# Kernel tuning notes

Hardware: AMD Instinct MI355X
Metric: run time of the kernel (lower is better)

## Reference

```python
import jax, jax.numpy as jnp
import numpy as np

K = 3          # kernel size (implied by 18/27 offset channels)
PAD = 1
STRIDE = 1


def setup_inputs() -> dict:
    key = jax.random.key(0)
    k0, k1, k2 = jax.random.split(key, 3)
    B, C, H, W = 4, 256, 64, 64
    Cout = 256
    x = jax.random.normal(k0, (B, C, H, W), jnp.float32)
    # offset/mask predicting conv: 18 offset + 9 mask channels (deform_group=1)
    w_off = jax.random.normal(k1, (27, C, K, K), jnp.float32) * 0.01
    b_off = jnp.zeros((27,), jnp.float32)
    # main deformable conv weight (bias=False)
    w = jax.random.normal(k2, (Cout, C, K, K), jnp.float32) * 0.05
    return {"x": x, "w_off": w_off, "b_off": b_off, "w": w}


def _modulated_dcn(x, w_off, b_off, w):
    B, C, H, W = x.shape
    KK = K * K
    # regular conv predicting offsets (+ mask)
    om = jax.lax.conv_general_dilated(
        x, w_off, (STRIDE, STRIDE), [(PAD, PAD), (PAD, PAD)],
        dimension_numbers=("NCHW", "OIHW", "NCHW")) + b_off[None, :, None, None]
    Ho, Wo = om.shape[2], om.shape[3]
    # channel layout: interleaved (dy, dx) per kernel tap, then 9 mask channels
    off = om[:, :2 * KK].reshape(B, KK, 2, Ho, Wo)
    mask = jax.nn.sigmoid(om[:, 2 * KK:3 * KK])            # (B, KK, Ho, Wo)

    ky, kx = jnp.meshgrid(jnp.arange(K), jnp.arange(K), indexing="ij")
    base_y = (jnp.arange(Ho) * STRIDE - PAD)[:, None]       # (Ho, 1)
    base_x = (jnp.arange(Wo) * STRIDE - PAD)[None, :]       # (1, Wo)
    # sampling positions p = p0 + pn + offset, shape (B, KK, Ho, Wo)
    py = base_y[None, None] + ky.reshape(KK)[None, :, None, None] + off[:, :, 0]
    px = base_x[None, None] + kx.reshape(KK)[None, :, None, None] + off[:, :, 1]

    y0f = jnp.floor(py)
    x0f = jnp.floor(px)
    ly = py - y0f
    lx = px - x0f
    y0 = y0f.astype(jnp.int32)
    x0 = x0f.astype(jnp.int32)

    xf = x.reshape(B, C, H * W)

    def samp(yi, xi):
        valid = ((yi >= 0) & (yi < H) & (xi >= 0) & (xi < W)).astype(x.dtype)
        idx = jnp.clip(yi, 0, H - 1) * W + jnp.clip(xi, 0, W - 1)
        v = jnp.take_along_axis(xf, idx.reshape(B, 1, -1), axis=2)
        return v.reshape(B, C, KK, Ho, Wo) * valid[:, None]

    # bilinear interpolation with zero padding outside the image
    v = (samp(y0,     x0    ) * ((1 - ly) * (1 - lx))[:, None]
         + samp(y0,     x0 + 1) * ((1 - ly) * lx)[:, None]
         + samp(y0 + 1, x0    ) * (ly * (1 - lx))[:, None]
         + samp(y0 + 1, x0 + 1) * (ly * lx)[:, None])
    v = v * mask[:, None]                                   # modulation
    # conv as contraction over (Cin, KK)
    return jnp.einsum("bckhw,ock->bohw", v, w.reshape(w.shape[0], C, KK))


def reference(x, w_off, b_off, w):
    return _modulated_dcn(x, w_off, b_off, w)
```

## Files before the change

### kernel.cpp

```cpp
#include <hip/hip_runtime.h>
#include <math.h>

#define HH 64
#define WW 64
#define CIN 256
#define COUT 256
#define KKT 9
#define HWSZ 4096
#define VP 260
#define TP 264

typedef __bf16  v8bf   __attribute__((ext_vector_type(8)));
typedef float   v4f    __attribute__((ext_vector_type(4)));
typedef short   short8 __attribute__((ext_vector_type(8)));
typedef unsigned short ushort4v __attribute__((ext_vector_type(4)));

__device__ inline unsigned short f2bf(float f) {
    union { float f; unsigned u; } uf; uf.f = f;
    unsigned r = uf.u + 0x7fff + ((uf.u >> 16) & 1);
    return (unsigned short)(r >> 16);
}
__device__ inline float bf2f(unsigned short u) {
    union { unsigned u; float f; } uf; uf.u = ((unsigned)u) << 16;
    return uf.f;
}

__global__ __launch_bounds__(256) void k_prep(const float* __restrict__ x,
                                              const float* __restrict__ w,
                                              const float* __restrict__ w_off,
                                              unsigned short* __restrict__ x_t,
                                              unsigned short* __restrict__ wprep,
                                              unsigned short* __restrict__ woffp) {
    __shared__ __align__(16) unsigned short s_t[32 * TP];
    int id  = blockIdx.x;
    int tid = threadIdx.x;
    if (id < 512) {
        int b    = id >> 7;
        int r    = id & 127;
        int h    = r >> 1;
        int half = r & 1;
        const float* xr = x + ((size_t)b * CIN) * HWSZ + h * WW + half * 32;
#pragma unroll
        for (int it = 0; it < 8; it++) {
            int idx = it * 256 + tid;
            int c   = idx >> 3;
            int p4  = idx & 7;
            float4 v = *(const float4*)(xr + (size_t)c * HWSZ + p4 * 4);
            s_t[(p4 * 4 + 0) * TP + c] = f2bf(v.x);
            s_t[(p4 * 4 + 1) * TP + c] = f2bf(v.y);
            s_t[(p4 * 4 + 2) * TP + c] = f2bf(v.z);
            s_t[(p4 * 4 + 3) * TP + c] = f2bf(v.w);
        }
        __syncthreads();
        unsigned short* orow = x_t + (((size_t)(b * 64 + h)) * WW + half * 32) * CIN;
#pragma unroll
        for (int it = 0; it < 4; it++) {
            int idx = it * 256 + tid;
            int px  = idx >> 5;
            int c8  = (idx & 31) * 8;
            *(short8*)(orow + (size_t)px * CIN + c8) = *(const short8*)&s_t[px * TP + c8];
        }
    } else if (id < 768) {
        float* s_w = (float*)s_t;
        int o = id - 512;
        for (int i = tid; i < 2304; i += 256) s_w[i] = w[(size_t)o * 2304 + i];
        __syncthreads();
        for (int u = tid; u < 576; u += 256) {
            int t  = u >> 3;
            int kq = u & 7;
            unsigned short v[4];
#pragma unroll
            for (int j = 0; j < 4; j++) {
                int kp = t * 32 + kq * 4 + j;
                int kk = kp >> 8;
                int c  = kp & 255;
                v[j] = f2bf(s_w[c * 9 + kk]);
            }
            *(ushort4v*)&wprep[((size_t)(t * 256 + o)) * 32 + kq * 4] = *(ushort4v*)v;
        }
    } else {
        int t = id - 768;
#pragma unroll
        for (int i = 0; i < 4; i++) {
            int idx = i * 256 + tid;
            int och = idx >> 5;
            int ki  = idx & 31;
            int kp  = t * 32 + ki;
            int kk  = kp >> 8;
            int c   = kp & 255;
            float v = (och < 27) ? w_off[((size_t)och * 256 + c) * 9 + kk] : 0.f;
            woffp[(size_t)t * 1024 + idx] = f2bf(v);
        }
    }
}

__global__ __launch_bounds__(256) void k_off_mfma(const unsigned short* __restrict__ x_t,
                                                  const unsigned short* __restrict__ woffp,
                                                  const float* __restrict__ b_off,
                                                  float* __restrict__ om) {
    int id    = blockIdx.x;
    int g     = id & 7;
    int phalf = (id >> 3) & 1;
    int hi    = (id >> 4) & 7;
    int b     = id >> 7;
    int h     = g * 8 + hi;
    int p0    = phalf * 32;
    int tid  = threadIdx.x;
    int lane = tid & 63;
    int wv   = tid >> 6;
    int g2   = wv >> 1;
    int ntw  = wv & 1;
    int m16  = lane & 15;
    int quad = lane >> 4;

    __shared__ unsigned short s_row[3 * 34 * VP];
    __shared__ float s_red[2][32][33];

    const unsigned short* xb = x_t + (size_t)b * HWSZ * CIN;

    for (int u = tid; u < 3 * 1088; u += 256) {
        int row = u / 1088;
        int rem = u - row * 1088;
        int px  = rem >> 5;
        int c8  = (rem & 31) * 8;
        int y   = h + row - 1;
        int xg  = p0 + px - 1;
        short8 val = (short8)0;
        if ((unsigned)y < HH && (unsigned)xg < WW)
            val = *(const short8*)(xb + ((size_t)y * WW + xg) * CIN + c8);
        *(short8*)&s_row[(row * 34 + px) * VP + c8] = val;
    }
    __syncthreads();

    v4f acc[2];
    acc[0] = (v4f)(0.f);
    acc[1] = (v4f)(0.f);

#pragma unroll
    for (int ky = 0; ky < 3; ky++) {
#pragma unroll
        for (int kx = 0; kx < 3; kx++) {
#pragma unroll
            for (int c2 = 0; c2 < 4; c2++) {
                int ch = c2 * 2 + g2;
                int t  = (ky * 3 + kx) * 8 + ch;
                const unsigned short* wp = woffp + (size_t)t * 1024;
                short8 af0 = *(const short8*)(wp + m16 * 32 + quad * 8);
                short8 af1 = *(const short8*)(wp + (16 + m16) * 32 + quad * 8);
                short8 bfr = *(const short8*)
                    &s_row[(ky * 34 + ntw * 16 + m16 + kx) * VP + ch * 32 + quad * 8];
                acc[0] = __builtin_amdgcn_mfma_f32_16x16x32_bf16(
                    __builtin_bit_cast(v8bf, af0), __builtin_bit_cast(v8bf, bfr), acc[0], 0, 0, 0);
                acc[1] = __builtin_amdgcn_mfma_f32_16x16x32_bf16(
                    __builtin_bit_cast(v8bf, af1), __builtin_bit_cast(v8bf, bfr), acc[1], 0, 0, 0);
            }
        }
    }

#pragma unroll
    for (int mt = 0; mt < 2; mt++)
#pragma unroll
        for (int r = 0; r < 4; r++)
            s_red[g2][mt * 16 + quad * 4 + r][ntw * 16 + m16] = acc[mt][r];
    __syncthreads();

    for (int i2 = tid; i2 < 27 * 32; i2 += 256) {
        int och = i2 >> 5;
        int px  = i2 & 31;
        float s = s_red[0][och][px] + s_red[1][och][px] + b_off[och];
        om[((size_t)b * 27 + och) * HWSZ + h * WW + p0 + px] = s;
    }
}

__global__ __launch_bounds__(512, 2) void k_main(const unsigned short* __restrict__ x_t,
                                                 const float* __restrict__ om,
                                                 const unsigned short* __restrict__ wprep,
                                                 float* __restrict__ out) {
    int id = blockIdx.x;
    id = ((id & 7) << 5) | (id >> 3);
    int b  = id >> 6;
    int h  = id & 63;
    int tid  = threadIdx.x;
    int lane = tid & 63;
    int oct  = tid >> 6;
    int m16  = lane & 15;
    int quad = lane >> 4;

    __shared__ int4   s_base[KKT][64];
    __shared__ float4 s_wt  [KKT][64];
    __shared__ __align__(16) unsigned short s_v[64 * VP];

    const float* omb = om + (size_t)b * 27 * HWSZ + h * WW;
    for (int i = tid; i < KKT * 64; i += 512) {
        int kk = i >> 6;
        int pl = i & 63;
        float offy = omb[(size_t)(2 * kk)     * HWSZ + pl];
        float offx = omb[(size_t)(2 * kk + 1) * HWSZ + pl];
        float mv   = omb[(size_t)(18 + kk)    * HWSZ + pl];
        int ky = kk / 3, kx = kk - 3 * (kk / 3);
        float py = (float)(h - 1 + ky) + offy;
        float px = (float)(pl - 1 + kx) + offx;
        float y0f = floorf(py);
        float x0f = floorf(px);
        float ly = py - y0f, lx = px - x0f;
        int y0 = (int)y0f, x0 = (int)x0f;
        float m = 1.f / (1.f + __expf(-mv));
        bool yv0 = (unsigned)y0       < HH;
        bool yv1 = (unsigned)(y0 + 1) < HH;
        bool xv0 = (unsigned)x0       < WW;
        bool xv1 = (unsigned)(x0 + 1) < WW;
        int y0c = min(max(y0, 0), HH - 1);
        int y1c = min(max(y0 + 1, 0), HH - 1);
        int x0c = min(max(x0, 0), WW - 1);
        int x1c = min(max(x0 + 1, 0), WW - 1);
        s_base[kk][pl] = make_int4((y0c * WW + x0c) * CIN, (y0c * WW + x1c) * CIN,
                                   (y1c * WW + x0c) * CIN, (y1c * WW + x1c) * CIN);
        s_wt[kk][pl] = make_float4(
            (yv0 && xv0) ? (1.f - ly) * (1.f - lx) * m : 0.f,
            (yv0 && xv1) ? (1.f - ly) * lx         * m : 0.f,
            (yv1 && xv0) ? ly * (1.f - lx)         * m : 0.f,
            (yv1 && xv1) ? ly * lx                 * m : 0.f);
    }
    __syncthreads();

    v4f acc[2][4];
#pragma unroll
    for (int mt = 0; mt < 2; mt++)
#pragma unroll
        for (int nt = 0; nt < 4; nt++) acc[mt][nt] = (v4f)(0.f);

    const unsigned short* xb = x_t + (size_t)b * HWSZ * CIN;
    const unsigned short* xc = xb + lane * 4;

    for (int kk = 0; kk < KKT; kk++) {
#pragma unroll
        for (int i = 0; i < 8; i++) {
            int pl = oct * 8 + i;
            int4   bp = s_base[kk][pl];
            float4 wt = s_wt[kk][pl];
            ushort4v t0 = *(const ushort4v*)(xc + bp.x);
            ushort4v t1 = *(const ushort4v*)(xc + bp.y);
            ushort4v t2 = *(const ushort4v*)(xc + bp.z);
            ushort4v t3 = *(const ushort4v*)(xc + bp.w);
            unsigned short vv[4];
#pragma unroll
            for (int j = 0; j < 4; j++) {
                float val = wt.x * bf2f(t0[j]) + wt.y * bf2f(t1[j])
                          + wt.z * bf2f(t2[j]) + wt.w * bf2f(t3[j]);
                vv[j] = f2bf(val);
            }
            *(ushort4v*)&s_v[pl * VP + lane * 4] = *(ushort4v*)vv;
        }
        __syncthreads();

#pragma unroll 2
        for (int ch = 0; ch < 8; ch++) {
            int t = kk * 8 + ch;
            const unsigned short* wp = wprep + ((size_t)t * 256 + oct * 32) * 32;
            short8 af0 = *(const short8*)(wp + m16 * 32 + quad * 8);
            short8 af1 = *(const short8*)(wp + (16 + m16) * 32 + quad * 8);
            short8 bfr[4];
#pragma unroll
            for (int nt = 0; nt < 4; nt++)
                bfr[nt] = *(const short8*)&s_v[(nt * 16 + m16) * VP + ch * 32 + quad * 8];
#pragma unroll
            for (int nt = 0; nt < 4; nt++) {
                acc[0][nt] = __builtin_amdgcn_mfma_f32_16x16x32_bf16(
                    __builtin_bit_cast(v8bf, af0), __builtin_bit_cast(v8bf, bfr[nt]),
                    acc[0][nt], 0, 0, 0);
                acc[1][nt] = __builtin_amdgcn_mfma_f32_16x16x32_bf16(
                    __builtin_bit_cast(v8bf, af1), __builtin_bit_cast(v8bf, bfr[nt]),
                    acc[1][nt], 0, 0, 0);
            }
        }
        __syncthreads();
    }

    float* ob = out + ((size_t)b * COUT) * HWSZ + h * WW;
#pragma unroll
    for (int mt = 0; mt < 2; mt++)
#pragma unroll
        for (int nt = 0; nt < 4; nt++)
#pragma unroll
            for (int r = 0; r < 4; r++) {
                int o = oct * 32 + mt * 16 + quad * 4 + r;
                ob[(size_t)o * HWSZ + nt * 16 + m16] = acc[mt][nt][r];
            }
}

extern "C" void kernel_launch(void* const* d_in, const int* in_sizes, int n_in,
                              void* d_out, int out_size, void* d_ws, size_t ws_size,
                              hipStream_t stream) {
    const float* x     = (const float*)d_in[0];
    const float* w_off = (const float*)d_in[1];
    const float* b_off = (const float*)d_in[2];
    const float* w     = (const float*)d_in[3];
    float* out = (float*)d_out;

    float* om = (float*)d_ws;
    unsigned short* x_t   = (unsigned short*)(om + 442368);
    unsigned short* wprep = x_t + (size_t)4 * HWSZ * CIN;
    unsigned short* woffp = wprep + 589824;

    hipLaunchKernelGGL(k_prep,     dim3(840), dim3(256), 0, stream, x, w, w_off, x_t, wprep, woffp);
    hipLaunchKernelGGL(k_off_mfma, dim3(512), dim3(256), 0, stream, x_t, woffp, b_off, om);
    hipLaunchKernelGGL(k_main,     dim3(256), dim3(512), 0, stream, x_t, om, wprep, out);
}
```

Before: 146.3 us.

## Double-buffer sampled tile and prefetch next tap gathers and weight fragments

Moves the bilinear gather loads for the next kernel tap ahead of the barrier into registers and double-buffers the shared sampled tile. This removes one of the two block barriers per tap. The weight A-fragments are also prefetched one chunk ahead. The aim is to hide global gather latency behind the MFMA phase, at the cost of many more live registers (32 ushort4 values plus prefetched fragments) and double the LDS for s_v, which may lower occupancy under launch_bounds(512,2).

```diff
diff --git a/kernel.cpp b/kernel.cpp
--- a/kernel.cpp
+++ b/kernel.cpp
@@ -188,7 +188,7 @@
 
     __shared__ int4   s_base[KKT][64];
     __shared__ float4 s_wt  [KKT][64];
-    __shared__ __align__(16) unsigned short s_v[64 * VP];
+    __shared__ __align__(16) unsigned short s_v[2][64 * VP];
 
     const float* omb = om + (size_t)b * 27 * HWSZ + h * WW;
     for (int i = tid; i < KKT * 64; i += 512) {
@@ -232,48 +232,75 @@
     const unsigned short* xb = x_t + (size_t)b * HWSZ * CIN;
     const unsigned short* xc = xb + lane * 4;
 
+    ushort4v tt[8][4];
+#pragma unroll
+    for (int i = 0; i < 8; i++) {
+        int4 bp = s_base[0][oct * 8 + i];
+        tt[i][0] = *(const ushort4v*)(xc + bp.x);
+        tt[i][1] = *(const ushort4v*)(xc + bp.y);
+        tt[i][2] = *(const ushort4v*)(xc + bp.z);
+        tt[i][3] = *(const ushort4v*)(xc + bp.w);
+    }
+
+#pragma unroll
     for (int kk = 0; kk < KKT; kk++) {
+        unsigned short* sv = &s_v[kk & 1][0];
+
 #pragma unroll
         for (int i = 0; i < 8; i++) {
             int pl = oct * 8 + i;
-            int4   bp = s_base[kk][pl];
             float4 wt = s_wt[kk][pl];
-            ushort4v t0 = *(const ushort4v*)(xc + bp.x);
-            ushort4v t1 = *(const ushort4v*)(xc + bp.y);
-            ushort4v t2 = *(const ushort4v*)(xc + bp.z);
-            ushort4v t3 = *(const ushort4v*)(xc + bp.w);
             unsigned short vv[4];
 #pragma unroll
             for (int j = 0; j < 4; j++) {
-                float val = wt.x * bf2f(t0[j]) + wt.y * bf2f(t1[j])
-                          + wt.z * bf2f(t2[j]) + wt.w * bf2f(t3[j]);
+                float val = wt.x * bf2f(tt[i][0][j]) + wt.y * bf2f(tt[i][1][j])
+                          + wt.z * bf2f(tt[i][2][j]) + wt.w * bf2f(tt[i][3][j]);
                 vv[j] = f2bf(val);
             }
-            *(ushort4v*)&s_v[pl * VP + lane * 4] = *(ushort4v*)vv;
-        }
-        __syncthreads();
-
-#pragma unroll 2
+            *(ushort4v*)&sv[pl * VP + lane * 4] = *(ushort4v*)vv;
+        }
+
+        if (kk < KKT - 1) {
+#pragma unroll
+            for (int i = 0; i < 8; i++) {
+                int4 bp = s_base[kk + 1][oct * 8 + i];
+                tt[i][0] = *(const ushort4v*)(xc + bp.x);
+                tt[i][1] = *(const ushort4v*)(xc + bp.y);
+                tt[i][2] = *(const ushort4v*)(xc + bp.z);
+                tt[i][3] = *(const ushort4v*)(xc + bp.w);
+            }
+        }
+        __builtin_amdgcn_sched_barrier(0);
+        asm volatile("s_waitcnt lgkmcnt(0)" ::: "memory");
+        __builtin_amdgcn_s_barrier();
+        __builtin_amdgcn_sched_barrier(0);
+
+        const unsigned short* wpb = wprep + ((size_t)(kk * 8) * 256 + oct * 32) * 32;
+        short8 a0 = *(const short8*)(wpb + m16 * 32 + quad * 8);
+        short8 a1 = *(const short8*)(wpb + (16 + m16) * 32 + quad * 8);
+#pragma unroll
         for (int ch = 0; ch < 8; ch++) {
-            int t = kk * 8 + ch;
-            const unsigned short* wp = wprep + ((size_t)t * 256 + oct * 32) * 32;
-            short8 af0 = *(const short8*)(wp + m16 * 32 + quad * 8);
-            short8 af1 = *(const short8*)(wp + (16 + m16) * 32 + quad * 8);
+            short8 na0, na1;
+            if (ch < 7) {
+                const unsigned short* wpn = wpb + (size_t)(ch + 1) * 8192;
+                na0 = *(const short8*)(wpn + m16 * 32 + quad * 8);
+                na1 = *(const short8*)(wpn + (16 + m16) * 32 + quad * 8);
+            }
             short8 bfr[4];
 #pragma unroll
             for (int nt = 0; nt < 4; nt++)
-                bfr[nt] = *(const short8*)&s_v[(nt * 16 + m16) * VP + ch * 32 + quad * 8];
+                bfr[nt] = *(const short8*)&sv[(nt * 16 + m16) * VP + ch * 32 + quad * 8];
 #pragma unroll
             for (int nt = 0; nt < 4; nt++) {
                 acc[0][nt] = __builtin_amdgcn_mfma_f32_16x16x32_bf16(
-                    __builtin_bit_cast(v8bf, af0), __builtin_bit_cast(v8bf, bfr[nt]),
+                    __builtin_bit_cast(v8bf, a0), __builtin_bit_cast(v8bf, bfr[nt]),
                     acc[0][nt], 0, 0, 0);
                 acc[1][nt] = __builtin_amdgcn_mfma_f32_16x16x32_bf16(
-                    __builtin_bit_cast(v8bf, af1), __builtin_bit_cast(v8bf, bfr[nt]),
+                    __builtin_bit_cast(v8bf, a1), __builtin_bit_cast(v8bf, bfr[nt]),
                     acc[1][nt], 0, 0, 0);
             }
-        }
-        __syncthreads();
+            if (ch < 7) { a0 = na0; a1 = na1; }
+        }
     }
 
     float* ob = out + ((size_t)b * COUT) * HWSZ + h * WW;
```

Measured after the change: 181.3 us. 1.24x slower.

## Split k_main tiles into half-rows with 16-byte bilinear gathers

Applied to the files above, without the earlier changes.

The main deformable-conv kernel now gives each block half an output row (32 pixels) instead of a full row, doubling the grid to 512 blocks and raising the occupancy hint to 4 blocks per CU. The gather stage is restructured so each lane loads 8 bf16 channels (16 bytes) per corner and handles two pixels per tap. Block-to-(batch, row) mapping is also changed for locality. This targets the low block count on a many-CU GPU, but the weight fragments loaded from global memory are now reused across only half as many pixels, doubling that traffic and adding more per-tap barrier overhead.

```diff
diff --git a/kernel.cpp b/kernel.cpp
--- a/kernel.cpp
+++ b/kernel.cpp
@@ -14,6 +14,7 @@
 typedef float   v4f    __attribute__((ext_vector_type(4)));
 typedef short   short8 __attribute__((ext_vector_type(8)));
 typedef unsigned short ushort4v __attribute__((ext_vector_type(4)));
+typedef unsigned short ushort8v __attribute__((ext_vector_type(8)));
 
 __device__ inline unsigned short f2bf(float f) {
     union { float f; unsigned u; } uf; uf.f = f;
@@ -172,34 +173,40 @@
     }
 }
 
-__global__ __launch_bounds__(512, 2) void k_main(const unsigned short* __restrict__ x_t,
+__global__ __launch_bounds__(512, 4) void k_main(const unsigned short* __restrict__ x_t,
                                                  const float* __restrict__ om,
                                                  const unsigned short* __restrict__ wprep,
                                                  float* __restrict__ out) {
-    int id = blockIdx.x;
-    id = ((id & 7) << 5) | (id >> 3);
-    int b  = id >> 6;
-    int h  = id & 63;
+    int id    = blockIdx.x;
+    int g     = id & 7;
+    int phalf = (id >> 3) & 1;
+    int hi    = (id >> 4) & 7;
+    int b     = id >> 7;
+    int h     = g * 8 + hi;
+    int p0    = phalf * 32;
     int tid  = threadIdx.x;
     int lane = tid & 63;
     int oct  = tid >> 6;
     int m16  = lane & 15;
     int quad = lane >> 4;
-
-    __shared__ int4   s_base[KKT][64];
-    __shared__ float4 s_wt  [KKT][64];
-    __shared__ __align__(16) unsigned short s_v[64 * VP];
+    int hsel = lane >> 5;
+    int l32  = lane & 31;
+
+    __shared__ int4   s_base[KKT][32];
+    __shared__ float4 s_wt  [KKT][32];
+    __shared__ __align__(16) unsigned short s_v[32 * VP];
 
     const float* omb = om + (size_t)b * 27 * HWSZ + h * WW;
-    for (int i = tid; i < KKT * 64; i += 512) {
-        int kk = i >> 6;
-        int pl = i & 63;
-        float offy = omb[(size_t)(2 * kk)     * HWSZ + pl];
-        float offx = omb[(size_t)(2 * kk + 1) * HWSZ + pl];
-        float mv   = omb[(size_t)(18 + kk)    * HWSZ + pl];
+    for (int i = tid; i < KKT * 32; i += 512) {
+        int kk = i >> 5;
+        int pl = i & 31;
+        int p  = p0 + pl;
+        float offy = omb[(size_t)(2 * kk)     * HWSZ + p];
+        float offx = omb[(size_t)(2 * kk + 1) * HWSZ + p];
+        float mv   = omb[(size_t)(18 + kk)    * HWSZ + p];
         int ky = kk / 3, kx = kk - 3 * (kk / 3);
         float py = (float)(h - 1 + ky) + offy;
-        float px = (float)(pl - 1 + kx) + offx;
+        float px = (float)(p - 1 + kx) + offx;
         float y0f = floorf(py);
         float x0f = floorf(px);
         float ly = py - y0f, lx = px - x0f;
@@ -223,33 +230,49 @@
     }
     __syncthreads();
 
-    v4f acc[2][4];
+    v4f acc[2][2];
 #pragma unroll
     for (int mt = 0; mt < 2; mt++)
 #pragma unroll
-        for (int nt = 0; nt < 4; nt++) acc[mt][nt] = (v4f)(0.f);
+        for (int nt = 0; nt < 2; nt++) acc[mt][nt] = (v4f)(0.f);
 
     const unsigned short* xb = x_t + (size_t)b * HWSZ * CIN;
-    const unsigned short* xc = xb + lane * 4;
+    const unsigned short* xcf = xb + l32 * 8;
 
     for (int kk = 0; kk < KKT; kk++) {
-#pragma unroll
-        for (int i = 0; i < 8; i++) {
-            int pl = oct * 8 + i;
-            int4   bp = s_base[kk][pl];
-            float4 wt = s_wt[kk][pl];
-            ushort4v t0 = *(const ushort4v*)(xc + bp.x);
-            ushort4v t1 = *(const ushort4v*)(xc + bp.y);
-            ushort4v t2 = *(const ushort4v*)(xc + bp.z);
-            ushort4v t3 = *(const ushort4v*)(xc + bp.w);
-            unsigned short vv[4];
-#pragma unroll
-            for (int j = 0; j < 4; j++) {
-                float val = wt.x * bf2f(t0[j]) + wt.y * bf2f(t1[j])
-                          + wt.z * bf2f(t2[j]) + wt.w * bf2f(t3[j]);
+        int pl0 = oct * 4 + hsel;
+        int pl1 = oct * 4 + 2 + hsel;
+        int4   bp0 = s_base[kk][pl0];
+        int4   bp1 = s_base[kk][pl1];
+        ushort8v ta0 = *(const ushort8v*)(xcf + bp0.x);
+        ushort8v ta1 = *(const ushort8v*)(xcf + bp0.y);
+        ushort8v ta2 = *(const ushort8v*)(xcf + bp0.z);
+        ushort8v ta3 = *(const ushort8v*)(xcf + bp0.w);
+        ushort8v tb0 = *(const ushort8v*)(xcf + bp1.x);
+        ushort8v tb1 = *(const ushort8v*)(xcf + bp1.y);
+        ushort8v tb2 = *(const ushort8v*)(xcf + bp1.z);
+        ushort8v tb3 = *(const ushort8v*)(xcf + bp1.w);
+        float4 wt0 = s_wt[kk][pl0];
+        float4 wt1 = s_wt[kk][pl1];
+        {
+            unsigned short vv[8];
+#pragma unroll
+            for (int j = 0; j < 8; j++) {
+                float val = wt0.x * bf2f(ta0[j]) + wt0.y * bf2f(ta1[j])
+                          + wt0.z * bf2f(ta2[j]) + wt0.w * bf2f(ta3[j]);
                 vv[j] = f2bf(val);
             }
-            *(ushort4v*)&s_v[pl * VP + lane * 4] = *(ushort4v*)vv;
+            *(ushort8v*)&s_v[pl0 * VP + l32 * 8] = *(ushort8v*)vv;
+        }
+        {
+            unsigned short vv[8];
+#pragma unroll
+            for (int j = 0; j < 8; j++) {
+                float val = wt1.x * bf2f(tb0[j]) + wt1.y * bf2f(tb1[j])
+                          + wt1.z * bf2f(tb2[j]) + wt1.w * bf2f(tb3[j]);
+                vv[j] = f2bf(val);
+            }
+            *(ushort8v*)&s_v[pl1 * VP + l32 * 8] = *(ushort8v*)vv;
         }
         __syncthreads();
 
@@ -259,12 +282,12 @@
             const unsigned short* wp = wprep + ((size_t)t * 256 + oct * 32) * 32;
             short8 af0 = *(const short8*)(wp + m16 * 32 + quad * 8);
             short8 af1 = *(const short8*)(wp + (16 + m16) * 32 + quad * 8);
-            short8 bfr[4];
-#pragma unroll
-            for (int nt = 0; nt < 4; nt++)
+            short8 bfr[2];
+#pragma unroll
+            for (int nt = 0; nt < 2; nt++)
                 bfr[nt] = *(const short8*)&s_v[(nt * 16 + m16) * VP + ch * 32 + quad * 8];
 #pragma unroll
-            for (int nt = 0; nt < 4; nt++) {
+            for (int nt = 0; nt < 2; nt++) {
                 acc[0][nt] = __builtin_amdgcn_mfma_f32_16x16x32_bf16(
                     __builtin_bit_cast(v8bf, af0), __builtin_bit_cast(v8bf, bfr[nt]),
                     acc[0][nt], 0, 0, 0);
@@ -276,11 +299,11 @@
         __syncthreads();
     }
 
-    float* ob = out + ((size_t)b * COUT) * HWSZ + h * WW;
+    float* ob = out + ((size_t)b * COUT) * HWSZ + h * WW + p0;
 #pragma unroll
     for (int mt = 0; mt < 2; mt++)
 #pragma unroll
-        for (int nt = 0; nt < 4; nt++)
+        for (int nt = 0; nt < 2; nt++)
 #pragma unroll
             for (int r = 0; r < 4; r++) {
                 int o = oct * 32 + mt * 16 + quad * 4 + r;
@@ -304,5 +327,5 @@
 
     hipLaunchKernelGGL(k_prep,     dim3(840), dim3(256), 0, stream, x, w, w_off, x_t, wprep, woffp);
     hipLaunchKernelGGL(k_off_mfma, dim3(512), dim3(256), 0, stream, x_t, woffp, b_off, om);
-    hipLaunchKernelGGL(k_main,     dim3(256), dim3(512), 0, stream, x_t, om, wprep, out);
-}
+    hipLaunchKernelGGL(k_main,     dim3(512), dim3(512), 0, stream, x_t, om, wprep, out);
+}
```

After: 139.7 us. 1.05x faster.
